# Optimization experiments

Measured on AMD Instinct MI355X. Metric: run time of the kernel, lower is better.

Reference implementation:

```python
import jax, jax.numpy as jnp
import numpy as np

D_MODEL, D_K, D_V = 1024, 64, 64
B, S = 2, 4096
NEG = 1e9


def setup_inputs() -> dict:
    key = jax.random.key(0)
    ks = jax.random.split(key, 10)
    Q = jax.random.normal(ks[0], (B, S, D_MODEL), dtype=jnp.float32)
    K = jax.random.normal(ks[1], (B, S, D_MODEL), dtype=jnp.float32)
    V = jax.random.normal(ks[2], (B, S, D_MODEL), dtype=jnp.float32)
    mask = jax.random.randint(ks[3], (B, S, S), 0, 2, dtype=jnp.int32)
    sc = 1.0 / np.sqrt(D_MODEL)
    Wq = jax.random.normal(ks[4], (D_K, D_MODEL), dtype=jnp.float32) * sc
    bq = jnp.zeros((D_K,), dtype=jnp.float32)
    Wk = jax.random.normal(ks[5], (D_K, D_MODEL), dtype=jnp.float32) * sc
    bk = jnp.zeros((D_K,), dtype=jnp.float32)
    Wv = jax.random.normal(ks[6], (D_V, D_MODEL), dtype=jnp.float32) * sc
    bv = jnp.zeros((D_V,), dtype=jnp.float32)
    return {"Q": Q, "K": K, "V": V, "mask": mask,
            "Wq": Wq, "bq": bq, "Wk": Wk, "bk": bk, "Wv": Wv, "bv": bv}


def reference(Q, K, V, mask, Wq, bq, Wk, bk, Wv, bv):
    # Linear projections: q,k -> [B,S,d_k], v -> [B,S,d_v]
    q = jnp.einsum('bsm,km->bsk', Q, Wq) + bq
    k = jnp.einsum('bsm,km->bsk', K, Wk) + bk
    v = jnp.einsum('bsm,vm->bsv', V, Wv) + bv
    # Scaled dot-product scores [B,S,S]
    x = jnp.einsum('bqk,bsk->bqs', q, k) / jnp.sqrt(jnp.float32(D_K))
    m = mask.astype(x.dtype)
    x = x * m - NEG * (1.0 - m)
    x = jax.nn.softmax(x, axis=2)
    y = jnp.einsum('bqs,bsv->bqv', x, v)
    return y
```

## Files before the change

kernel.cpp:

```cpp
#include <hip/hip_runtime.h>

typedef unsigned short u16;
typedef __bf16 bf16x8 __attribute__((ext_vector_type(8)));
typedef float f32x4 __attribute__((ext_vector_type(4)));

#define MFMA16(a, b, c) __builtin_amdgcn_mfma_f32_16x16x32_bf16((a), (b), (c), 0, 0, 0)

__device__ __forceinline__ bf16x8 ld8(const u16* p) {
    return *reinterpret_cast<const bf16x8*>(p);
}

__device__ __forceinline__ unsigned pk2(float a, float b) {
    unsigned short ua = __builtin_bit_cast(unsigned short, (__bf16)a);
    unsigned short ub = __builtin_bit_cast(unsigned short, (__bf16)b);
    return (unsigned)ua | ((unsigned)ub << 16);
}

__device__ __forceinline__ bf16x8 cvt8(float4 a, float4 b) {
    bf16x8 r;
    r[0] = (__bf16)a.x; r[1] = (__bf16)a.y; r[2] = (__bf16)a.z; r[3] = (__bf16)a.w;
    r[4] = (__bf16)b.x; r[5] = (__bf16)b.y; r[6] = (__bf16)b.z; r[7] = (__bf16)b.w;
    return r;
}

__global__ __launch_bounds__(256) void wcvt_kernel(
    const float* __restrict__ Wq, const float* __restrict__ Wk,
    const float* __restrict__ Wv, u16* __restrict__ wb)
{
    const int t = blockIdx.x * 256 + threadIdx.x;
    const int mat = t >> 13;
    const int idx = (t & 8191) * 8;
    const float* src = (mat == 0) ? Wq : (mat == 1) ? Wk : Wv;
    float4 a = *(const float4*)(src + idx);
    float4 b = *(const float4*)(src + idx + 4);
    uint4 o;
    o.x = pk2(a.x, a.y); o.y = pk2(a.z, a.w);
    o.z = pk2(b.x, b.y); o.w = pk2(b.z, b.w);
    *reinterpret_cast<uint4*>(wb + (size_t)mat * 65536 + idx) = o;
}

__global__ __launch_bounds__(256) void proj_kernel(
    const float* __restrict__ Q, const float* __restrict__ K, const float* __restrict__ V,
    const float* __restrict__ bq, const float* __restrict__ bk, const float* __restrict__ bv,
    const u16* __restrict__ wb, u16* __restrict__ qb, u16* __restrict__ kb,
    u16* __restrict__ vtb)
{
    const int mat  = blockIdx.x >> 7;
    const int tile = blockIdx.x & 127;
    const int lane = threadIdx.x & 63;
    const int w    = threadIdx.x >> 6;
    const int c    = lane & 15, g = lane >> 4;

    const float* X = (mat == 0) ? Q : (mat == 1) ? K : V;
    const u16*   W = wb + (size_t)mat * 65536;

    const int rw = tile * 64 + w * 16;
    const float* xp = X + (size_t)(rw + c) * 1024 + g * 8;
    const u16*   wp = W + (size_t)c * 1024 + g * 8;

    f32x4 acc[4] = {};
    float4 xa = *(const float4*)xp;
    float4 xb = *(const float4*)(xp + 4);

    #pragma unroll 2
    for (int kk = 0; kk < 32; ++kk) {
        bf16x8 a = cvt8(xa, xb);
        if (kk < 31) {
            xa = *(const float4*)(xp + (kk + 1) * 32);
            xb = *(const float4*)(xp + (kk + 1) * 32 + 4);
        }
        const u16* wk = wp + kk * 32;
        if (mat < 2) {
            #pragma unroll
            for (int t = 0; t < 4; ++t)
                acc[t] = MFMA16(a, ld8(wk + t * 16 * 1024), acc[t]);
        } else {
            #pragma unroll
            for (int t = 0; t < 4; ++t)
                acc[t] = MFMA16(ld8(wk + t * 16 * 1024), a, acc[t]);
        }
    }

    if (mat < 2) {
        const float* bias = (mat == 0) ? bq : bk;
        u16* dst = (mat == 0) ? qb : kb;
        #pragma unroll
        for (int t = 0; t < 4; ++t) {
            const float bz = bias[t * 16 + c];
            #pragma unroll
            for (int r = 0; r < 4; ++r) {
                const int row = rw + g * 4 + r;
                dst[(size_t)row * 64 + t * 16 + c] =
                    __builtin_bit_cast(u16, (__bf16)(acc[t][r] + bz));
            }
        }
    } else {
        const int sg = rw + c;
        const int bidx = sg >> 12, sin = sg & 4095;
        #pragma unroll
        for (int t = 0; t < 4; ++t) {
            #pragma unroll
            for (int r = 0; r < 4; ++r) {
                const int dv = t * 16 + g * 4 + r;
                vtb[(size_t)(bidx * 64 + dv) * 4096 + sin] =
                    __builtin_bit_cast(u16, (__bf16)(acc[t][r] + bv[dv]));
            }
        }
    }
}

__global__ __launch_bounds__(256) void attn_kernel(
    const int* __restrict__ mask, const u16* __restrict__ qb,
    const u16* __restrict__ kb, const u16* __restrict__ vtb,
    float* __restrict__ pacc, float* __restrict__ pm, float* __restrict__ pl)
{
    __shared__ uint2 plds[4][128];
    const int lane = threadIdx.x & 63, w = threadIdx.x >> 6;
    const int c = lane & 15, g = lane >> 4;
    const int gw    = blockIdx.x * 4 + w;
    const int strip = gw >> 3;
    const int chunk = gw & 7;
    const int b     = strip >> 8;
    const int q0    = (strip & 255) * 16;
    const int sBase = chunk * 512;
    const float SSC = 0.18033688011112042f;

    const u16* qrow = qb + (size_t)((b << 12) + q0 + c) * 64 + g * 8;
    const bf16x8 qf0 = ld8(qrow);
    const bf16x8 qf1 = ld8(qrow + 32);

    const u16* kbase = kb  + ((size_t)b << 12) * 64;
    const u16* vbase = vtb + (size_t)(b * 64 + c) * 4096;
    const int* mrow  = mask + ((size_t)b << 24) + (size_t)(q0 + c) * 4096 + g * 4;

    f32x4 acc0 = {}, acc1 = {}, acc2 = {}, acc3 = {};
    const f32x4 zf = {};
    float m_run = -__builtin_inff(), l_run = 0.f;

    int4 mk0 = *(const int4*)(mrow + sBase);
    int4 mk1 = *(const int4*)(mrow + sBase + 16);

    for (int it = 0; it < 16; ++it) {
        const int s0 = sBase + it * 32;
        const u16* kp0 = kbase + (size_t)(s0 + c) * 64 + g * 8;
        const u16* kp1 = kp0 + 16 * 64;
        f32x4 d0 = MFMA16(ld8(kp0), qf0, zf);
        d0 = MFMA16(ld8(kp0 + 32), qf1, d0);
        f32x4 d1 = MFMA16(ld8(kp1), qf0, zf);
        d1 = MFMA16(ld8(kp1 + 32), qf1, d1);

        const int4 cm0 = mk0, cm1 = mk1;
        if (it < 15) {
            mk0 = *(const int4*)(mrow + s0 + 32);
            mk1 = *(const int4*)(mrow + s0 + 48);
        }

        const float x0 = cm0.x ? d0[0] * SSC : -1e9f;
        const float x1 = cm0.y ? d0[1] * SSC : -1e9f;
        const float x2 = cm0.z ? d0[2] * SSC : -1e9f;
        const float x3 = cm0.w ? d0[3] * SSC : -1e9f;
        const float x4 = cm1.x ? d1[0] * SSC : -1e9f;
        const float x5 = cm1.y ? d1[1] * SSC : -1e9f;
        const float x6 = cm1.z ? d1[2] * SSC : -1e9f;
        const float x7 = cm1.w ? d1[3] * SSC : -1e9f;

        float tm = fmaxf(fmaxf(fmaxf(x0, x1), fmaxf(x2, x3)),
                         fmaxf(fmaxf(x4, x5), fmaxf(x6, x7)));
        tm = fmaxf(tm, __shfl_xor(tm, 16));
        tm = fmaxf(tm, __shfl_xor(tm, 32));
        const float m_new = fmaxf(m_run, tm);
        const float f = exp2f(m_run - m_new);

        const float p0 = exp2f(x0 - m_new), p1 = exp2f(x1 - m_new);
        const float p2 = exp2f(x2 - m_new), p3 = exp2f(x3 - m_new);
        const float p4 = exp2f(x4 - m_new), p5 = exp2f(x5 - m_new);
        const float p6 = exp2f(x6 - m_new), p7 = exp2f(x7 - m_new);
        float rs = ((p0 + p1) + (p2 + p3)) + ((p4 + p5) + (p6 + p7));
        rs += __shfl_xor(rs, 16);
        rs += __shfl_xor(rs, 32);
        l_run = l_run * f + rs;
        m_run = m_new;

        plds[w][c * 8 + ( g      ^ (c & 7))] = make_uint2(pk2(p0, p1), pk2(p2, p3));
        plds[w][c * 8 + ((g + 4) ^ (c & 7))] = make_uint2(pk2(p4, p5), pk2(p6, p7));

        if (__any(f < 1.0f)) {
            const float f0 = __shfl(f, g * 4 + 0);
            const float f1 = __shfl(f, g * 4 + 1);
            const float f2 = __shfl(f, g * 4 + 2);
            const float f3 = __shfl(f, g * 4 + 3);
            acc0[0] *= f0; acc0[1] *= f1; acc0[2] *= f2; acc0[3] *= f3;
            acc1[0] *= f0; acc1[1] *= f1; acc1[2] *= f2; acc1[3] *= f3;
            acc2[0] *= f0; acc2[1] *= f1; acc2[2] *= f2; acc2[3] *= f3;
            acc3[0] *= f0; acc3[1] *= f1; acc3[2] *= f2; acc3[3] *= f3;
        }

        union { uint2 u[2]; bf16x8 v; } pa;
        pa.u[0] = plds[w][c * 8 + ((2 * g    ) ^ (c & 7))];
        pa.u[1] = plds[w][c * 8 + ((2 * g + 1) ^ (c & 7))];

        const u16* vp = vbase + s0 + g * 8;
        acc0 = MFMA16(pa.v, ld8(vp),             acc0);
        acc1 = MFMA16(pa.v, ld8(vp + 16 * 4096), acc1);
        acc2 = MFMA16(pa.v, ld8(vp + 32 * 4096), acc2);
        acc3 = MFMA16(pa.v, ld8(vp + 48 * 4096), acc3);
    }

    const size_t pidx = (size_t)(strip * 8 + chunk) * 16;
    #pragma unroll
    for (int r = 0; r < 4; ++r) {
        const size_t row = pidx + g * 4 + r;
        pacc[row * 64 +  0 + c] = acc0[r];
        pacc[row * 64 + 16 + c] = acc1[r];
        pacc[row * 64 + 32 + c] = acc2[r];
        pacc[row * 64 + 48 + c] = acc3[r];
    }
    if (lane < 16) {
        pm[pidx + c] = m_run;
        pl[pidx + c] = l_run;
    }
}

__global__ __launch_bounds__(256) void comb_kernel(
    const float* __restrict__ pacc, const float* __restrict__ pm,
    const float* __restrict__ pl, float* __restrict__ out)
{
    const int t = blockIdx.x * 256 + threadIdx.x;
    const int r = t >> 6, dv = t & 63;
    const int strip = r >> 4, qi = r & 15;
    const int base = strip * 128 + qi;
    float mv[8];
    float M = -__builtin_inff();
    #pragma unroll
    for (int cc = 0; cc < 8; ++cc) { mv[cc] = pm[base + cc * 16]; M = fmaxf(M, mv[cc]); }
    float num = 0.f, den = 0.f;
    #pragma unroll
    for (int cc = 0; cc < 8; ++cc) {
        const float wgt = exp2f(mv[cc] - M);
        num += wgt * pacc[(size_t)(base + cc * 16) * 64 + dv];
        den += wgt * pl[base + cc * 16];
    }
    out[t] = num / den;
}

extern "C" void kernel_launch(void* const* d_in, const int* in_sizes, int n_in,
                              void* d_out, int out_size, void* d_ws, size_t ws_size,
                              hipStream_t stream)
{
    const float* Q    = (const float*)d_in[0];
    const float* K    = (const float*)d_in[1];
    const float* V    = (const float*)d_in[2];
    const int*   mask = (const int*)d_in[3];
    const float* Wq   = (const float*)d_in[4];
    const float* bq   = (const float*)d_in[5];
    const float* Wk   = (const float*)d_in[6];
    const float* bk   = (const float*)d_in[7];
    const float* Wv   = (const float*)d_in[8];
    const float* bv   = (const float*)d_in[9];
    float* out = (float*)d_out;

    char* ws = (char*)d_ws;
    u16*   wb   = (u16*)(ws);
    u16*   qb   = (u16*)(ws + 393216);
    u16*   kb   = (u16*)(ws + 393216 + 1048576);
    u16*   vtb  = (u16*)(ws + 393216 + 2097152);
    float* pacc = (float*)(ws + 4194304);
    float* pm   = (float*)(ws + 4194304 + 16777216);
    float* pl   = (float*)(ws + 4194304 + 16777216 + 262144);

    wcvt_kernel<<<96, 256, 0, stream>>>(Wq, Wk, Wv, wb);
    proj_kernel<<<384, 256, 0, stream>>>(Q, K, V, bq, bk, bv, wb, qb, kb, vtb);
    attn_kernel<<<1024, 256, 0, stream>>>(mask, qb, kb, vtb, pacc, pm, pl);
    comb_kernel<<<2048, 256, 0, stream>>>(pacc, pm, pl, out);
}
```

Measured before the change: 139.9 us.

## Pack attention mask into bitfields during projection and prefetch K/V tiles

```diff
diff --git a/kernel.cpp b/kernel.cpp
--- a/kernel.cpp
+++ b/kernel.cpp
@@ -1,6 +1,7 @@
 #include <hip/hip_runtime.h>
 
 typedef unsigned short u16;
+typedef unsigned long long u64;
 typedef __bf16 bf16x8 __attribute__((ext_vector_type(8)));
 typedef float f32x4 __attribute__((ext_vector_type(4)));
 
@@ -39,17 +40,47 @@
     *reinterpret_cast<uint4*>(wb + (size_t)mat * 65536 + idx) = o;
 }
 
-__global__ __launch_bounds__(256) void proj_kernel(
+__global__ __launch_bounds__(256) void projpack_kernel(
     const float* __restrict__ Q, const float* __restrict__ K, const float* __restrict__ V,
     const float* __restrict__ bq, const float* __restrict__ bk, const float* __restrict__ bv,
-    const u16* __restrict__ wb, u16* __restrict__ qb, u16* __restrict__ kb,
-    u16* __restrict__ vtb)
-{
+    const u16* __restrict__ wb, const int* __restrict__ mask,
+    u16* __restrict__ qb, u16* __restrict__ kb, u16* __restrict__ vtb,
+    u64* __restrict__ bits64)
+{
+    const int lane = threadIdx.x & 63;
+    const int w    = threadIdx.x >> 6;
+
+    if (blockIdx.x >= 384) {
+        const int gwv = (blockIdx.x - 384) * 4 + w;
+        const int* mp = mask + (size_t)gwv * 4096 + lane;
+        u64* op = bits64 + (size_t)gwv * 64;
+        #pragma unroll 1
+        for (int step = 0; step < 8; ++step) {
+            const int* sp = mp + step * 512;
+            const u64 b0 = __ballot(sp[0]   != 0);
+            const u64 b1 = __ballot(sp[64]  != 0);
+            const u64 b2 = __ballot(sp[128] != 0);
+            const u64 b3 = __ballot(sp[192] != 0);
+            const u64 b4 = __ballot(sp[256] != 0);
+            const u64 b5 = __ballot(sp[320] != 0);
+            const u64 b6 = __ballot(sp[384] != 0);
+            const u64 b7 = __ballot(sp[448] != 0);
+            u64 mine = b0;
+            if (lane == 1) mine = b1;
+            if (lane == 2) mine = b2;
+            if (lane == 3) mine = b3;
+            if (lane == 4) mine = b4;
+            if (lane == 5) mine = b5;
+            if (lane == 6) mine = b6;
+            if (lane == 7) mine = b7;
+            if (lane < 8) op[step * 8 + lane] = mine;
+        }
+        return;
+    }
+
     const int mat  = blockIdx.x >> 7;
     const int tile = blockIdx.x & 127;
-    const int lane = threadIdx.x & 63;
-    const int w    = threadIdx.x >> 6;
-    const int c    = lane & 15, g = lane >> 4;
+    const int c = lane & 15, g = lane >> 4;
 
     const float* X = (mat == 0) ? Q : (mat == 1) ? K : V;
     const u16*   W = wb + (size_t)mat * 65536;
@@ -110,7 +141,7 @@
 }
 
 __global__ __launch_bounds__(256) void attn_kernel(
-    const int* __restrict__ mask, const u16* __restrict__ qb,
+    const unsigned* __restrict__ bits, const u16* __restrict__ qb,
     const u16* __restrict__ kb, const u16* __restrict__ vtb,
     float* __restrict__ pacc, float* __restrict__ pm, float* __restrict__ pl)
 {
@@ -129,40 +160,49 @@
     const bf16x8 qf0 = ld8(qrow);
     const bf16x8 qf1 = ld8(qrow + 32);
 
-    const u16* kbase = kb  + ((size_t)b << 12) * 64;
-    const u16* vbase = vtb + (size_t)(b * 64 + c) * 4096;
-    const int* mrow  = mask + ((size_t)b << 24) + (size_t)(q0 + c) * 4096 + g * 4;
+    const u16* kfp = kb  + (((size_t)b << 12) + sBase + c) * 64 + g * 8;
+    const u16* vfp = vtb + (size_t)(b * 64 + c) * 4096 + sBase + g * 8;
+    const unsigned* brow = bits + (size_t)((b << 12) + q0 + c) * 128 + (sBase >> 5);
 
     f32x4 acc0 = {}, acc1 = {}, acc2 = {}, acc3 = {};
     const f32x4 zf = {};
     float m_run = -__builtin_inff(), l_run = 0.f;
 
-    int4 mk0 = *(const int4*)(mrow + sBase);
-    int4 mk1 = *(const int4*)(mrow + sBase + 16);
-
+    unsigned wA = brow[0], wB = brow[1];
+    bf16x8 k00 = ld8(kfp),            k01 = ld8(kfp + 32);
+    bf16x8 k10 = ld8(kfp + 16 * 64),  k11 = ld8(kfp + 16 * 64 + 32);
+
+    #pragma unroll 1
     for (int it = 0; it < 16; ++it) {
-        const int s0 = sBase + it * 32;
-        const u16* kp0 = kbase + (size_t)(s0 + c) * 64 + g * 8;
-        const u16* kp1 = kp0 + 16 * 64;
-        f32x4 d0 = MFMA16(ld8(kp0), qf0, zf);
-        d0 = MFMA16(ld8(kp0 + 32), qf1, d0);
-        f32x4 d1 = MFMA16(ld8(kp1), qf0, zf);
-        d1 = MFMA16(ld8(kp1 + 32), qf1, d1);
-
-        const int4 cm0 = mk0, cm1 = mk1;
-        if (it < 15) {
-            mk0 = *(const int4*)(mrow + s0 + 32);
-            mk1 = *(const int4*)(mrow + s0 + 48);
-        }
-
-        const float x0 = cm0.x ? d0[0] * SSC : -1e9f;
-        const float x1 = cm0.y ? d0[1] * SSC : -1e9f;
-        const float x2 = cm0.z ? d0[2] * SSC : -1e9f;
-        const float x3 = cm0.w ? d0[3] * SSC : -1e9f;
-        const float x4 = cm1.x ? d1[0] * SSC : -1e9f;
-        const float x5 = cm1.y ? d1[1] * SSC : -1e9f;
-        const float x6 = cm1.z ? d1[2] * SSC : -1e9f;
-        const float x7 = cm1.w ? d1[3] * SSC : -1e9f;
+        const u16* vp = vfp + it * 32;
+        const bf16x8 v0 = ld8(vp);
+        const bf16x8 v1 = ld8(vp + 16 * 4096);
+        const bf16x8 v2 = ld8(vp + 32 * 4096);
+        const bf16x8 v3 = ld8(vp + 48 * 4096);
+
+        f32x4 d0 = MFMA16(k00, qf0, zf);
+        d0 = MFMA16(k01, qf1, d0);
+        f32x4 d1 = MFMA16(k10, qf0, zf);
+        d1 = MFMA16(k11, qf1, d1);
+
+        const int no = (it < 15) ? (it + 1) * 2048 : it * 2048;
+        k00 = ld8(kfp + no);            k01 = ld8(kfp + no + 32);
+        k10 = ld8(kfp + no + 16 * 64);  k11 = ld8(kfp + no + 16 * 64 + 32);
+
+        const unsigned wc_ = wA;
+        wA = wB;
+        wB = brow[(it + 2 < 16) ? (it + 2) : 15];
+
+        const unsigned s0b = wc_ >> (g * 4);
+        const unsigned s1b = wc_ >> (16 + g * 4);
+        const float x0 = (s0b & 1u) ? d0[0] * SSC : -1e9f;
+        const float x1 = (s0b & 2u) ? d0[1] * SSC : -1e9f;
+        const float x2 = (s0b & 4u) ? d0[2] * SSC : -1e9f;
+        const float x3 = (s0b & 8u) ? d0[3] * SSC : -1e9f;
+        const float x4 = (s1b & 1u) ? d1[0] * SSC : -1e9f;
+        const float x5 = (s1b & 2u) ? d1[1] * SSC : -1e9f;
+        const float x6 = (s1b & 4u) ? d1[2] * SSC : -1e9f;
+        const float x7 = (s1b & 8u) ? d1[3] * SSC : -1e9f;
 
         float tm = fmaxf(fmaxf(fmaxf(x0, x1), fmaxf(x2, x3)),
                          fmaxf(fmaxf(x4, x5), fmaxf(x6, x7)));
@@ -199,11 +239,10 @@
         pa.u[0] = plds[w][c * 8 + ((2 * g    ) ^ (c & 7))];
         pa.u[1] = plds[w][c * 8 + ((2 * g + 1) ^ (c & 7))];
 
-        const u16* vp = vbase + s0 + g * 8;
-        acc0 = MFMA16(pa.v, ld8(vp),             acc0);
-        acc1 = MFMA16(pa.v, ld8(vp + 16 * 4096), acc1);
-        acc2 = MFMA16(pa.v, ld8(vp + 32 * 4096), acc2);
-        acc3 = MFMA16(pa.v, ld8(vp + 48 * 4096), acc3);
+        acc0 = MFMA16(pa.v, v0, acc0);
+        acc1 = MFMA16(pa.v, v1, acc1);
+        acc2 = MFMA16(pa.v, v2, acc2);
+        acc3 = MFMA16(pa.v, v3, acc3);
     }
 
     const size_t pidx = (size_t)(strip * 8 + chunk) * 16;
@@ -264,12 +303,14 @@
     u16*   qb   = (u16*)(ws + 393216);
     u16*   kb   = (u16*)(ws + 393216 + 1048576);
     u16*   vtb  = (u16*)(ws + 393216 + 2097152);
-    float* pacc = (float*)(ws + 4194304);
-    float* pm   = (float*)(ws + 4194304 + 16777216);
-    float* pl   = (float*)(ws + 4194304 + 16777216 + 262144);
+    u64*   bits = (u64*)(ws + 4194304);
+    float* pm   = (float*)(ws + 8388608);
+    float* pl   = (float*)(ws + 8388608 + 262144);
+    float* pacc = (float*)(ws + 8388608 + 524288);
 
     wcvt_kernel<<<96, 256, 0, stream>>>(Wq, Wk, Wv, wb);
-    proj_kernel<<<384, 256, 0, stream>>>(Q, K, V, bq, bk, bv, wb, qb, kb, vtb);
-    attn_kernel<<<1024, 256, 0, stream>>>(mask, qb, kb, vtb, pacc, pm, pl);
+    projpack_kernel<<<2432, 256, 0, stream>>>(Q, K, V, bq, bk, bv, wb, mask,
+                                              qb, kb, vtb, bits);
+    attn_kernel<<<1024, 256, 0, stream>>>((const unsigned*)bits, qb, kb, vtb, pacc, pm, pl);
     comb_kernel<<<2048, 256, 0, stream>>>(pacc, pm, pl, out);
 }
```

Result: no change. 137.6 us (-1.6%).
